# Performance work log

Measured on AMD Instinct MI355X. Metric: run time of the kernel, lower is better.

Reference implementation:

```python
import jax, jax.numpy as jnp
import numpy as np

B, T, DS, N, DR, H, DF, NK, HID = 4, 1024, 1024, 16, 256, 4, 1024, 3, 128
K_VALUES = (1, 2, 4)  # k_values for max_k=4


def _ln(x, scale, bias):
    mu = jnp.mean(x, axis=-1, keepdims=True)
    var = jnp.var(x, axis=-1, keepdims=True)
    return (x - mu) * jax.lax.rsqrt(var + 1e-5) * scale + bias


def setup_inputs() -> dict:
    key = jax.random.key(0)
    ks = jax.random.split(key, 16)
    p = lambda k, shp: 0.02 * jax.random.normal(k, shp, dtype=jnp.float32)
    return {
        "s": jax.random.normal(ks[0], (B, T, DS), dtype=jnp.float32),
        "r": jax.random.normal(ks[1], (B, T, N, DR), dtype=jnp.float32),
        # DifficultyEstimator MLP (d_s -> 128 -> 3 k-logits)
        "Wd1": p(ks[2], (DS, HID)), "bd1": jnp.zeros((HID,), jnp.float32),
        "Wd2": p(ks[3], (HID, NK)), "bd2": jnp.zeros((NK,), jnp.float32),
        # SlotAllocator (r -> hidden -> 1, plus surface projection)
        "Wa1": p(ks[4], (DR, HID)), "ba1": jnp.zeros((HID,), jnp.float32),
        "Wa2": p(ks[5], (HID, 1)), "ba2": jnp.zeros((1,), jnp.float32),
        "Ws": p(ks[6], (DS, 1)),
        # ReasoningStream: masked slot self-attention + FFN
        "ln1_s": jnp.ones((DR,), jnp.float32), "ln1_b": jnp.zeros((DR,), jnp.float32),
        "Wq": p(ks[7], (DR, DR)), "Wk": p(ks[8], (DR, DR)),
        "Wv": p(ks[9], (DR, DR)), "Wo": p(ks[10], (DR, DR)),
        "ln2_s": jnp.ones((DR,), jnp.float32), "ln2_b": jnp.zeros((DR,), jnp.float32),
        "Wf1": p(ks[11], (DR, DF)), "bf1": jnp.zeros((DF,), jnp.float32),
        "Wf2": p(ks[12], (DF, DR)), "bf2": jnp.zeros((DR,), jnp.float32),
    }


def _reasoning_step(r, mask, ln1_s, ln1_b, Wq, Wk, Wv, Wo, ln2_s, ln2_b, Wf1, bf1, Wf2, bf2):
    # one masked update of the per-position slot set: (B,T,N,DR)
    Dh = DR // H
    h = _ln(r, ln1_s, ln1_b)
    q = (h @ Wq).reshape(*h.shape[:-1], H, Dh)
    k = (h @ Wk).reshape(*h.shape[:-1], H, Dh)
    v = (h @ Wv).reshape(*h.shape[:-1], H, Dh)
    scores = jnp.einsum("btnhd,btmhd->bthnm", q, k) / jnp.sqrt(jnp.float32(Dh))
    attn = jax.nn.softmax(scores, axis=-1)
    o = jnp.einsum("bthnm,btmhd->btnhd", attn, v).reshape(r.shape) @ Wo
    r = r + mask * o
    h2 = _ln(r, ln2_s, ln2_b)
    ffn = jax.nn.gelu(h2 @ Wf1 + bf1) @ Wf2 + bf2
    return r + mask * ffn


def reference(s, r, Wd1, bd1, Wd2, bd2, Wa1, ba1, Wa2, ba2, Ws,
              ln1_s, ln1_b, Wq, Wk, Wv, Wo, ln2_s, ln2_b, Wf1, bf1, Wf2, bf2):
    # SlotAllocator: per-position per-slot soft mask (B,T,N,1)
    slot_mask = jax.nn.sigmoid(
        (jax.nn.relu(r @ Wa1 + ba1) @ Wa2 + ba2) + (s @ Ws)[:, :, None, :]
    )
    # DifficultyEstimator: k logits / weights per position (B,T,3)
    k_logits = jax.nn.relu(s @ Wd1 + bd1) @ Wd2 + bd2
    probs = jax.nn.softmax(k_logits, axis=-1)
    k_weights = probs
    # routing balance loss: mse of mean probs vs uniform
    mean_probs = probs.mean(axis=(0, 1))
    routing_loss = jnp.mean((mean_probs - 1.0 / NK) ** 2)
    k_tensor = jnp.asarray(K_VALUES, dtype=s.dtype)
    mean_k = (probs * k_tensor).sum(axis=-1).mean()
    # _combine_adaptive_reasoning (training path): run max_k steps, keep
    # candidates at k in K_VALUES, weighted combine per position.
    step_params = (ln1_s, ln1_b, Wq, Wk, Wv, Wo, ln2_s, ln2_b, Wf1, bf1, Wf2, bf2)
    candidates = []
    r_step = r
    for step in range(1, max(K_VALUES) + 1):
        r_step = _reasoning_step(r_step, slot_mask, *step_params)
        if step in K_VALUES:
            candidates.append(r_step)
    stacked = jnp.stack(candidates, axis=2)  # (B,T,3,N,DR)
    r_out = (k_weights[..., None, None] * stacked).sum(axis=2)
    return r_out, routing_loss, mean_k
```

## Files before the change

kernel.cpp:

```cpp
#include <hip/hip_runtime.h>
#include <hip/hip_bf16.h>
#include <math.h>


#define NPOS 4096
#define R_ELEMS 16777216ull
#define NB 384

typedef __attribute__((ext_vector_type(8))) short short8;
typedef __attribute__((ext_vector_type(4))) float f32x4;

#define MF(a, b, c) __builtin_amdgcn_mfma_f32_16x16x32_bf16(a, b, c, 0, 0, 0)

__device__ __forceinline__ short bf16rne(float f) {
  union { float f; unsigned u; } v; v.f = f;
  unsigned r = v.u + 0x7FFFu + ((v.u >> 16) & 1u);
  return (short)(r >> 16);
}

__device__ __forceinline__ short bf16c(float f) {
  __hip_bfloat16 h = __float2bfloat16(f);
  return *reinterpret_cast<short*>(&h);
}

__device__ __forceinline__ float fast_gelu(float x) {
  float x2 = x * x;
  float z = 0.7978845608028654f * x * (1.f + 0.044715f * x2);
  float e = __expf(2.f * z);
  float t = 1.f - 2.f * __builtin_amdgcn_rcpf(e + 1.f);
  return 0.5f * x * (1.f + t);
}

__global__ void pack_weight(const float* __restrict__ W, short* __restrict__ P,
                            int K, int N) {
  int id = blockIdx.x * 256 + threadIdx.x;
  int KC = K >> 5, T = N >> 4;
  if (id >= T * KC * 64) return;
  int l = id & 63, kc = (id >> 6) % KC, t = id / (64 * KC);
  int g = l >> 4, n = l & 15;
  short8 o;
#pragma unroll
  for (int jj = 0; jj < 8; jj++) {
    int k = 32 * kc + 4 * g + (jj & 3) + 16 * (jj >> 2);
    o[jj] = bf16rne(W[(size_t)k * N + 16 * t + n]);
  }
  *(short8*)(P + (size_t)id * 8) = o;
}

__global__ void pack_stream(const float* __restrict__ Wq, const float* __restrict__ Wk,
                            const float* __restrict__ Wv, const float* __restrict__ Wo,
                            const float* __restrict__ Wf1, const float* __restrict__ Wf2,
                            short* __restrict__ S) {
  int id = blockIdx.x * 256 + threadIdx.x;
  int f = id >> 6, lane = id & 63;
  if (f >= 1536) return;
  const float* W; int ldN, t, kc;
  if (f < 384) {
    int hh = f / 96, rem = f % 96, mat = rem / 32, r2 = rem % 32;
    t = 4 * hh + r2 / 8; kc = r2 % 8; ldN = 256;
    W = (mat == 0) ? Wq : (mat == 1) ? Wk : Wv;
  } else if (f < 512) {
    int gg = f - 384; t = gg / 8; kc = gg % 8; ldN = 256; W = Wo;
  } else {
    int gg = f - 512, hc = gg / 32, r2 = gg % 32;
    if (r2 < 16) { W = Wf1; ldN = 1024; t = 2 * hc + r2 / 8; kc = r2 % 8; }
    else         { W = Wf2; ldN = 256;  t = r2 - 16;         kc = hc;    }
  }
  int g = lane >> 4, n = lane & 15;
  short8 o;
#pragma unroll
  for (int jj = 0; jj < 8; jj++) {
    int k = 32 * kc + 4 * g + (jj & 3) + 16 * (jj >> 2);
    o[jj] = bf16rne(W[(size_t)k * ldN + 16 * t + n]);
  }
  *(short8*)(S + (size_t)f * 512 + lane * 8) = o;
}

__device__ __forceinline__ short8 ldfrag(const short* __restrict__ P, int t, int kc,
                                         int KC, int lane) {
  return *(const short8*)(P + ((size_t)((t * KC + kc) * 64 + lane) << 3));
}

__global__ void init_accum_kernel(float* accum) {
  if (threadIdx.x < 4) accum[threadIdx.x] = 0.f;
}

__global__ void sproj_kernel(const float* __restrict__ s, const float* __restrict__ Ws,
                             float* __restrict__ sproj) {
  int p = blockIdx.x, tid = threadIdx.x;
  const float* row = s + (size_t)p * 1024;
  float sum = 0.f;
#pragma unroll
  for (int k0 = 0; k0 < 1024; k0 += 256) sum += row[k0 + tid] * Ws[k0 + tid];
#pragma unroll
  for (int m = 1; m < 64; m <<= 1) sum += __shfl_xor(sum, m, 64);
  __shared__ float red[4];
  if ((tid & 63) == 0) red[tid >> 6] = sum;
  __syncthreads();
  if (tid == 0) sproj[p] = red[0] + red[1] + red[2] + red[3];
}

__global__ void difficulty_mfma(const float* __restrict__ s, const short* __restrict__ PWd1,
                                const float* __restrict__ bd1, const float* __restrict__ Wd2,
                                const float* __restrict__ bd2, float* __restrict__ probsv,
                                float* __restrict__ accum) {
  int tid = threadIdx.x;
  int wave = tid >> 6, lane = tid & 63, n = lane & 15, g = lane >> 4;
  int p0 = (blockIdx.x * 4 + wave) * 16;
  const float* sg = s + (size_t)(p0 + n) * 1024;
  f32x4 ha[8];
  const f32x4 Z = {0.f, 0.f, 0.f, 0.f};
#pragma unroll
  for (int t = 0; t < 8; t++) ha[t] = Z;
  for (int kc = 0; kc < 32; kc++) {
    f32x4 x0 = *(const f32x4*)(sg + 32 * kc + 4 * g);
    f32x4 x1 = *(const f32x4*)(sg + 32 * kc + 16 + 4 * g);
    short8 sb;
#pragma unroll
    for (int c = 0; c < 4; c++) { sb[c] = bf16c(x0[c]); sb[c + 4] = bf16c(x1[c]); }
#pragma unroll
    for (int t = 0; t < 8; t++) ha[t] = MF(ldfrag(PWd1, t, kc, 32, lane), sb, ha[t]);
  }
  float v0 = 0.f, v1 = 0.f, v2 = 0.f;
#pragma unroll
  for (int t = 0; t < 8; t++)
#pragma unroll
    for (int c = 0; c < 4; c++) {
      int hid = 16 * t + 4 * g + c;
      float u = fmaxf(ha[t][c] + bd1[hid], 0.f);
      v0 += u * Wd2[hid * 3 + 0];
      v1 += u * Wd2[hid * 3 + 1];
      v2 += u * Wd2[hid * 3 + 2];
    }
  v0 += __shfl_xor(v0, 16, 64); v0 += __shfl_xor(v0, 32, 64);
  v1 += __shfl_xor(v1, 16, 64); v1 += __shfl_xor(v1, 32, 64);
  v2 += __shfl_xor(v2, 16, 64); v2 += __shfl_xor(v2, 32, 64);
  if (g == 0) {
    float l0 = v0 + bd2[0], l1 = v1 + bd2[1], l2 = v2 + bd2[2];
    float mx = fmaxf(l0, fmaxf(l1, l2));
    float e0 = __expf(l0 - mx), e1 = __expf(l1 - mx), e2 = __expf(l2 - mx);
    float inv = 1.f / (e0 + e1 + e2);
    float p0v = e0 * inv, p1v = e1 * inv, p2v = e2 * inv;
    int p = p0 + n;
    probsv[p * 3 + 0] = p0v; probsv[p * 3 + 1] = p1v; probsv[p * 3 + 2] = p2v;
    atomicAdd(accum + 0, p0v);
    atomicAdd(accum + 1, p1v);
    atomicAdd(accum + 2, p2v);
    atomicAdd(accum + 3, p0v * 1.f + p1v * 2.f + p2v * 4.f);
  }
}

__global__ void slot_mask_mfma(const float* __restrict__ r, const short* __restrict__ PWa1,
                               const float* __restrict__ ba1, const float* __restrict__ Wa2,
                               const float* __restrict__ ba2, const float* __restrict__ sproj,
                               float* __restrict__ mask) {
  int tid = threadIdx.x;
  int wave = tid >> 6, lane = tid & 63, n = lane & 15, g = lane >> 4;
  int p = blockIdx.x * 4 + wave;
  const float* rsg = r + (size_t)p * 4096 + n * 256;
  short8 rb[8];
#pragma unroll
  for (int kc = 0; kc < 8; kc++) {
    f32x4 x0 = *(const f32x4*)(rsg + 32 * kc + 4 * g);
    f32x4 x1 = *(const f32x4*)(rsg + 32 * kc + 16 + 4 * g);
    short8 o;
#pragma unroll
    for (int c = 0; c < 4; c++) { o[c] = bf16c(x0[c]); o[c + 4] = bf16c(x1[c]); }
    rb[kc] = o;
  }
  f32x4 ha[8];
  const f32x4 Z = {0.f, 0.f, 0.f, 0.f};
#pragma unroll
  for (int t = 0; t < 8; t++) ha[t] = Z;
#pragma unroll
  for (int kc = 0; kc < 8; kc++)
#pragma unroll
    for (int t = 0; t < 8; t++) ha[t] = MF(ldfrag(PWa1, t, kc, 8, lane), rb[kc], ha[t]);
  float v = 0.f;
#pragma unroll
  for (int t = 0; t < 8; t++)
#pragma unroll
    for (int c = 0; c < 4; c++) {
      int hid = 16 * t + 4 * g + c;
      v += fmaxf(ha[t][c] + ba1[hid], 0.f) * Wa2[hid];
    }
  v += __shfl_xor(v, 16, 64);
  v += __shfl_xor(v, 32, 64);
  if (g == 0) mask[p * 16 + n] = 1.f / (1.f + __expf(-(v + ba2[0] + sproj[p])));
}

__global__ __launch_bounds__(256, 2) void reason_all(
    const float* __restrict__ r_src, const float* __restrict__ maskg,
    const float* __restrict__ probsv, float* __restrict__ outp,
    const short* __restrict__ Wstream,
    const float* __restrict__ ln1s, const float* __restrict__ ln1b,
    const float* __restrict__ ln2s, const float* __restrict__ ln2b,
    const float* __restrict__ bf1g, const float* __restrict__ bf2g) {
  __shared__ __align__(16) short Wbuf[4 * 8192];
  __shared__ __align__(16) float P_ln1s[256], P_ln1b[256], P_ln2s[256], P_ln2b[256];
  __shared__ __align__(16) float P_bf1[1024], P_bf2[256];
  const int tid = threadIdx.x;
  P_ln1s[tid] = ln1s[tid]; P_ln1b[tid] = ln1b[tid];
  P_ln2s[tid] = ln2s[tid]; P_ln2b[tid] = ln2b[tid];
  P_bf2[tid] = bf2g[tid];
  for (int i = tid; i < 1024; i += 256) P_bf1[i] = bf1g[i];
  __syncthreads();

  const int wave = tid >> 6, lane = tid & 63;
  const int n = lane & 15, g = lane >> 4;
  const int p = blockIdx.x * 4 + wave;
  const size_t base = (size_t)p * 4096;
  const f32x4 Z = {0.f, 0.f, 0.f, 0.f};

  auto stage_issue = [&](int c) {
    const short* gs = Wstream + (size_t)(c % 96) * 8192 + wave * 2048 + lane * 8;
    short* ld = (short*)Wbuf + (c & 3) * 8192 + wave * 2048;
#pragma unroll
    for (int i = 0; i < 4; ++i)
      __builtin_amdgcn_global_load_lds(
          (const __attribute__((address_space(1))) void*)(gs + i * 512),
          (__attribute__((address_space(3))) void*)(ld + i * 512), 16, 0, 0);
  };
  stage_issue(0); stage_issue(1); stage_issue(2);

  f32x4 r0[8], r1[8];
  {
    const float* rsg = r_src + base + n * 256;
#pragma unroll
    for (int kc = 0; kc < 8; kc++) {
      r0[kc] = *(const f32x4*)(rsg + 32 * kc + 4 * g);
      r1[kc] = *(const f32x4*)(rsg + 32 * kc + 16 + 4 * g);
    }
  }
  const float maskn = maskg[p * 16 + n];
  const float w0 = probsv[p * 3 + 0];
  const float w1 = probsv[p * 3 + 1];
  const float w2 = probsv[p * 3 + 2];

  int cidx = 0;
  auto boundary = [&]() -> const short* {
    int c = cidx++;
    if (c <= NB - 3)
      asm volatile("s_waitcnt vmcnt(8) lgkmcnt(0)\ns_barrier" ::: "memory");
    else if (c == NB - 2)
      asm volatile("s_waitcnt vmcnt(4) lgkmcnt(0)\ns_barrier" ::: "memory");
    else
      asm volatile("s_waitcnt vmcnt(0) lgkmcnt(0)\ns_barrier" ::: "memory");
    __builtin_amdgcn_sched_barrier(0);
    if (c + 3 < NB) stage_issue(c + 3);
    return &Wbuf[(c & 3) * 8192];
  };
#define FRAG(Bp, i) (*(const short8*)((Bp) + (i) * 512 + lane * 8))

  short8 h1[8];
  auto do_ln = [&](const float* sc, const float* bi) {
    float sum = 0.f, sq = 0.f;
#pragma unroll
    for (int kc = 0; kc < 8; kc++)
#pragma unroll
      for (int c = 0; c < 4; c++) {
        sum += r0[kc][c] + r1[kc][c];
        sq += r0[kc][c] * r0[kc][c] + r1[kc][c] * r1[kc][c];
      }
    sum += __shfl_xor(sum, 16, 64); sq += __shfl_xor(sq, 16, 64);
    sum += __shfl_xor(sum, 32, 64); sq += __shfl_xor(sq, 32, 64);
    float mu = sum * (1.f / 256.f);
    float inv = rsqrtf(sq * (1.f / 256.f) - mu * mu + 1e-5f);
#pragma unroll
    for (int kc = 0; kc < 8; kc++) {
      f32x4 s0 = *(const f32x4*)&sc[32 * kc + 4 * g];
      f32x4 b0 = *(const f32x4*)&bi[32 * kc + 4 * g];
      f32x4 s1 = *(const f32x4*)&sc[32 * kc + 16 + 4 * g];
      f32x4 b1 = *(const f32x4*)&bi[32 * kc + 16 + 4 * g];
      short8 hh;
#pragma unroll
      for (int c = 0; c < 4; c++) {
        hh[c]     = bf16c((r0[kc][c] - mu) * inv * s0[c] + b0[c]);
        hh[c + 4] = bf16c((r1[kc][c] - mu) * inv * s1[c] + b1[c]);
      }
      h1[kc] = hh;
    }
  };

  for (int sidx = 0; sidx < 4; ++sidx) {
    do_ln(P_ln1s, P_ln1b);

    short8 ob[8];
#pragma unroll
    for (int hh = 0; hh < 4; hh++) {
      short8 qb[2], kb[2];
      f32x4 va[4];
      {
        f32x4 qa[4];
#pragma unroll
        for (int tp = 0; tp < 2; tp++) {
          const short* B = boundary();
          qa[2 * tp] = Z; qa[2 * tp + 1] = Z;
          __builtin_amdgcn_s_setprio(1);
#pragma unroll
          for (int tt = 0; tt < 2; tt++)
#pragma unroll
            for (int kc = 0; kc < 8; kc++)
              qa[2 * tp + tt] = MF(FRAG(B, tt * 8 + kc), h1[kc], qa[2 * tp + tt]);
          __builtin_amdgcn_s_setprio(0);
        }
#pragma unroll
        for (int c = 0; c < 2; c++) {
          short8 x;
#pragma unroll
          for (int jj = 0; jj < 8; jj++) x[jj] = bf16c(qa[2 * c + (jj >> 2)][jj & 3]);
          qb[c] = x;
        }
      }
      {
        f32x4 ka[4];
#pragma unroll
        for (int tp = 0; tp < 2; tp++) {
          const short* B = boundary();
          ka[2 * tp] = Z; ka[2 * tp + 1] = Z;
          __builtin_amdgcn_s_setprio(1);
#pragma unroll
          for (int tt = 0; tt < 2; tt++)
#pragma unroll
            for (int kc = 0; kc < 8; kc++)
              ka[2 * tp + tt] = MF(FRAG(B, tt * 8 + kc), h1[kc], ka[2 * tp + tt]);
          __builtin_amdgcn_s_setprio(0);
        }
#pragma unroll
        for (int c = 0; c < 2; c++) {
          short8 x;
#pragma unroll
          for (int jj = 0; jj < 8; jj++) x[jj] = bf16c(ka[2 * c + (jj >> 2)][jj & 3]);
          kb[c] = x;
        }
      }
#pragma unroll
      for (int tp = 0; tp < 2; tp++) {
        const short* B = boundary();
        va[2 * tp] = Z; va[2 * tp + 1] = Z;
        __builtin_amdgcn_s_setprio(1);
#pragma unroll
        for (int tt = 0; tt < 2; tt++)
#pragma unroll
          for (int kc = 0; kc < 8; kc++)
            va[2 * tp + tt] = MF(h1[kc], FRAG(B, tt * 8 + kc), va[2 * tp + tt]);
        __builtin_amdgcn_s_setprio(0);
      }
      f32x4 sc = Z;
      sc = MF(kb[0], qb[0], sc);
      sc = MF(kb[1], qb[1], sc);
#pragma unroll
      for (int c = 0; c < 4; c++) sc[c] *= 0.125f;
      float mx = fmaxf(fmaxf(sc[0], sc[1]), fmaxf(sc[2], sc[3]));
      mx = fmaxf(mx, __shfl_xor(mx, 16, 64));
      mx = fmaxf(mx, __shfl_xor(mx, 32, 64));
      float e0 = __expf(sc[0] - mx), e1 = __expf(sc[1] - mx);
      float e2 = __expf(sc[2] - mx), e3 = __expf(sc[3] - mx);
      float sm = e0 + e1 + e2 + e3;
      sm += __shfl_xor(sm, 16, 64);
      sm += __shfl_xor(sm, 32, 64);
      float isv = __builtin_amdgcn_rcpf(sm);
      short8 pb;
      pb[0] = bf16c(e0 * isv); pb[1] = bf16c(e1 * isv);
      pb[2] = bf16c(e2 * isv); pb[3] = bf16c(e3 * isv);
      pb[4] = 0; pb[5] = 0; pb[6] = 0; pb[7] = 0;
      short8 vb[4];
#pragma unroll
      for (int t = 0; t < 4; t++) {
        short8 x;
        x[0] = bf16c(va[t][0]); x[1] = bf16c(va[t][1]);
        x[2] = bf16c(va[t][2]); x[3] = bf16c(va[t][3]);
        x[4] = 0; x[5] = 0; x[6] = 0; x[7] = 0;
        vb[t] = x;
      }
      f32x4 oh[4];
#pragma unroll
      for (int t = 0; t < 4; t++) { oh[t] = Z; oh[t] = MF(vb[t], pb, oh[t]); }
#pragma unroll
      for (int c = 0; c < 2; c++) {
        short8 x;
#pragma unroll
        for (int jj = 0; jj < 8; jj++)
          x[jj] = bf16c(maskn * oh[2 * c + (jj >> 2)][jj & 3]);
        ob[2 * hh + c] = x;
      }
    }

#pragma unroll
    for (int kk = 0; kk < 8; kk++) {
      const short* B = boundary();
      __builtin_amdgcn_s_setprio(1);
#pragma unroll
      for (int kc = 0; kc < 8; kc++) r0[kk] = MF(FRAG(B, kc), ob[kc], r0[kk]);
#pragma unroll
      for (int kc = 0; kc < 8; kc++) r1[kk] = MF(FRAG(B, 8 + kc), ob[kc], r1[kk]);
      __builtin_amdgcn_s_setprio(0);
    }

    do_ln(P_ln2s, P_ln2b);
#pragma unroll 1
    for (int hc = 0; hc < 32; hc++) {
      f32x4 ht0 = Z, ht1 = Z;
      {
        const short* B = boundary();
        __builtin_amdgcn_s_setprio(1);
#pragma unroll
        for (int kc = 0; kc < 8; kc++) ht0 = MF(FRAG(B, kc), h1[kc], ht0);
#pragma unroll
        for (int kc = 0; kc < 8; kc++) ht1 = MF(FRAG(B, 8 + kc), h1[kc], ht1);
        __builtin_amdgcn_s_setprio(0);
      }
      f32x4 u0 = *(const f32x4*)&P_bf1[32 * hc + 4 * g];
      f32x4 u1 = *(const f32x4*)&P_bf1[32 * hc + 16 + 4 * g];
      short8 hbb;
#pragma unroll
      for (int c = 0; c < 4; c++) {
        hbb[c]     = bf16c(maskn * fast_gelu(ht0[c] + u0[c]));
        hbb[c + 4] = bf16c(maskn * fast_gelu(ht1[c] + u1[c]));
      }
      {
        const short* B = boundary();
        __builtin_amdgcn_s_setprio(1);
#pragma unroll
        for (int tt = 0; tt < 8; tt++) {
          r0[tt] = MF(FRAG(B, 2 * tt), hbb, r0[tt]);
          r1[tt] = MF(FRAG(B, 2 * tt + 1), hbb, r1[tt]);
        }
        __builtin_amdgcn_s_setprio(0);
      }
    }
#pragma unroll
    for (int kc = 0; kc < 8; kc++) {
      f32x4 b0 = *(const f32x4*)&P_bf2[32 * kc + 4 * g];
      f32x4 b1 = *(const f32x4*)&P_bf2[32 * kc + 16 + 4 * g];
#pragma unroll
      for (int c = 0; c < 4; c++) {
        r0[kc][c] += maskn * b0[c];
        r1[kc][c] += maskn * b1[c];
      }
    }

    if (sidx == 0) {
      float* op = outp + base + n * 256;
#pragma unroll
      for (int kc = 0; kc < 8; kc++) {
        f32x4 o0, o1;
#pragma unroll
        for (int c = 0; c < 4; c++) { o0[c] = w0 * r0[kc][c]; o1[c] = w0 * r1[kc][c]; }
        *(f32x4*)(op + 32 * kc + 4 * g) = o0;
        *(f32x4*)(op + 32 * kc + 16 + 4 * g) = o1;
      }
    } else if (sidx == 1 || sidx == 3) {
      float wc = (sidx == 1) ? w1 : w2;
      float* op = outp + base + n * 256;
#pragma unroll
      for (int kc = 0; kc < 8; kc++) {
        f32x4 o0 = *(f32x4*)(op + 32 * kc + 4 * g);
        f32x4 o1 = *(f32x4*)(op + 32 * kc + 16 + 4 * g);
#pragma unroll
        for (int c = 0; c < 4; c++) { o0[c] += wc * r0[kc][c]; o1[c] += wc * r1[kc][c]; }
        *(f32x4*)(op + 32 * kc + 4 * g) = o0;
        *(f32x4*)(op + 32 * kc + 16 + 4 * g) = o1;
      }
    }
  }
}

__global__ void finalize_kernel(const float* __restrict__ accum, float* __restrict__ dst) {
  const float inv = 1.f / 4096.f;
  float m0 = accum[0] * inv, m1 = accum[1] * inv, m2 = accum[2] * inv;
  const float u = 1.f / 3.f;
  float d0 = m0 - u, d1 = m1 - u, d2 = m2 - u;
  dst[0] = (d0 * d0 + d1 * d1 + d2 * d2) * (1.f / 3.f);
  dst[1] = accum[3] * inv;
}

extern "C" void kernel_launch(void* const* d_in, const int* in_sizes, int n_in,
                              void* d_out, int out_size, void* d_ws, size_t ws_size,
                              hipStream_t stream) {
  const float* s    = (const float*)d_in[0];
  const float* r    = (const float*)d_in[1];
  const float* Wd1  = (const float*)d_in[2];
  const float* bd1  = (const float*)d_in[3];
  const float* Wd2  = (const float*)d_in[4];
  const float* bd2  = (const float*)d_in[5];
  const float* Wa1  = (const float*)d_in[6];
  const float* ba1  = (const float*)d_in[7];
  const float* Wa2  = (const float*)d_in[8];
  const float* ba2  = (const float*)d_in[9];
  const float* Wsp  = (const float*)d_in[10];
  const float* ln1s = (const float*)d_in[11];
  const float* ln1b = (const float*)d_in[12];
  const float* Wq   = (const float*)d_in[13];
  const float* Wk   = (const float*)d_in[14];
  const float* Wv   = (const float*)d_in[15];
  const float* Wo   = (const float*)d_in[16];
  const float* ln2s = (const float*)d_in[17];
  const float* ln2b = (const float*)d_in[18];
  const float* Wf1  = (const float*)d_in[19];
  const float* bf1  = (const float*)d_in[20];
  const float* Wf2  = (const float*)d_in[21];
  const float* bf2  = (const float*)d_in[22];

  float* out = (float*)d_out;
  float* wsf = (float*)d_ws;
  float* mask   = wsf;
  float* sproj  = wsf + 65536;
  float* probsv = wsf + 65536 + 4096;
  float* accum  = wsf + 65536 + 4096 + 12288;
  short* pk     = (short*)(wsf + 131072);
  short* Wstream = pk;
  short* PWa1    = pk + 786432;
  short* PWd1    = pk + 819200;

  pack_stream<<<384, 256, 0, stream>>>(Wq, Wk, Wv, Wo, Wf1, Wf2, Wstream);
  pack_weight<<<16, 256, 0, stream>>>(Wa1, PWa1, 256, 128);
  pack_weight<<<64, 256, 0, stream>>>(Wd1, PWd1, 1024, 128);

  init_accum_kernel<<<1, 64, 0, stream>>>(accum);
  sproj_kernel<<<NPOS, 256, 0, stream>>>(s, Wsp, sproj);
  difficulty_mfma<<<64, 256, 0, stream>>>(s, PWd1, bd1, Wd2, bd2, probsv, accum);
  slot_mask_mfma<<<NPOS / 4, 256, 0, stream>>>(r, PWa1, ba1, Wa2, ba2, sproj, mask);

  reason_all<<<NPOS / 4, 256, 0, stream>>>(r, mask, probsv, out, Wstream,
                                           ln1s, ln1b, ln2s, ln2b, bf1, bf2);

  finalize_kernel<<<1, 1, 0, stream>>>(accum, out + R_ELEMS);
}
```

Baseline: 705.4 us.

## Process two positions per wave to reuse each staged weight fragment twice

Each wave now handles two positions (A and B) and applies every LDS weight fragment to both, which halves the grid and the total weight streaming through LDS per position. The Wo projection is interleaved per head, with the weight stream reordered to match, so the attention output can be consumed right after each head instead of buffering all heads. This doubles the accumulator register footprint (four r arrays), which can cut occupancy or cause spills, and the loops are left at unroll 1.

```diff
diff --git a/kernel.cpp b/kernel.cpp
--- a/kernel.cpp
+++ b/kernel.cpp
@@ -55,16 +55,24 @@
   int f = id >> 6, lane = id & 63;
   if (f >= 1536) return;
   const float* W; int ldN, t, kc;
-  if (f < 384) {
-    int hh = f / 96, rem = f % 96, mat = rem / 32, r2 = rem % 32;
-    t = 4 * hh + r2 / 8; kc = r2 % 8; ldN = 256;
-    W = (mat == 0) ? Wq : (mat == 1) ? Wk : Wv;
-  } else if (f < 512) {
-    int gg = f - 384; t = gg / 8; kc = gg % 8; ldN = 256; W = Wo;
+  if (f < 512) {
+    int head = f >> 7, rem = f & 127;
+    if (rem < 96) {
+      int mat = rem / 32, r2 = rem % 32;
+      t = 4 * head + (r2 >> 3);
+      kc = r2 & 7; ldN = 256;
+      W = (mat == 0) ? Wq : (mat == 1) ? Wk : Wv;
+    } else {
+      int r2 = rem - 96;
+      int ch = r2 >> 4, floc = r2 & 15;
+      t = ch * 8 + (floc >> 1);
+      kc = 2 * head + (floc & 1);
+      ldN = 256; W = Wo;
+    }
   } else {
     int gg = f - 512, hc = gg / 32, r2 = gg % 32;
-    if (r2 < 16) { W = Wf1; ldN = 1024; t = 2 * hc + r2 / 8; kc = r2 % 8; }
-    else         { W = Wf2; ldN = 256;  t = r2 - 16;         kc = hc;    }
+    if (r2 < 16) { W = Wf1; ldN = 1024; t = 2 * hc + (r2 >> 3); kc = r2 & 7; }
+    else         { W = Wf2; ldN = 256;  t = r2 - 16;            kc = hc;    }
   }
   int g = lane >> 4, n = lane & 15;
   short8 o;
@@ -208,8 +216,8 @@
 
   const int wave = tid >> 6, lane = tid & 63;
   const int n = lane & 15, g = lane >> 4;
-  const int p = blockIdx.x * 4 + wave;
-  const size_t base = (size_t)p * 4096;
+  const int pA = blockIdx.x * 8 + wave * 2, pB = pA + 1;
+  const size_t baseA = (size_t)pA * 4096, baseB = (size_t)pB * 4096;
   const f32x4 Z = {0.f, 0.f, 0.f, 0.f};
 
   auto stage_issue = [&](int c) {
@@ -223,19 +231,20 @@
   };
   stage_issue(0); stage_issue(1); stage_issue(2);
 
-  f32x4 r0[8], r1[8];
+  f32x4 rA0[8], rA1[8], rB0[8], rB1[8];
   {
-    const float* rsg = r_src + base + n * 256;
+    const float* ra = r_src + baseA + n * 256;
+    const float* rb = r_src + baseB + n * 256;
 #pragma unroll
     for (int kc = 0; kc < 8; kc++) {
-      r0[kc] = *(const f32x4*)(rsg + 32 * kc + 4 * g);
-      r1[kc] = *(const f32x4*)(rsg + 32 * kc + 16 + 4 * g);
-    }
-  }
-  const float maskn = maskg[p * 16 + n];
-  const float w0 = probsv[p * 3 + 0];
-  const float w1 = probsv[p * 3 + 1];
-  const float w2 = probsv[p * 3 + 2];
+      rA0[kc] = *(const f32x4*)(ra + 32 * kc + 4 * g);
+      rA1[kc] = *(const f32x4*)(ra + 32 * kc + 16 + 4 * g);
+      rB0[kc] = *(const f32x4*)(rb + 32 * kc + 4 * g);
+      rB1[kc] = *(const f32x4*)(rb + 32 * kc + 16 + 4 * g);
+    }
+  }
+  const float maskA = maskg[pA * 16 + n];
+  const float maskB = maskg[pB * 16 + n];
 
   int cidx = 0;
   auto boundary = [&]() -> const short* {
@@ -252,8 +261,9 @@
   };
 #define FRAG(Bp, i) (*(const short8*)((Bp) + (i) * 512 + lane * 8))
 
-  short8 h1[8];
-  auto do_ln = [&](const float* sc, const float* bi) {
+  short8 hA[8], hB[8];
+  auto do_ln = [&](const f32x4* r0, const f32x4* r1, const float* sc,
+                   const float* bi, short8* h) {
     float sum = 0.f, sq = 0.f;
 #pragma unroll
     for (int kc = 0; kc < 8; kc++)
@@ -278,153 +288,197 @@
         hh[c]     = bf16c((r0[kc][c] - mu) * inv * s0[c] + b0[c]);
         hh[c + 4] = bf16c((r1[kc][c] - mu) * inv * s1[c] + b1[c]);
       }
-      h1[kc] = hh;
+      h[kc] = hh;
     }
   };
 
+#pragma unroll 1
   for (int sidx = 0; sidx < 4; ++sidx) {
-    do_ln(P_ln1s, P_ln1b);
-
-    short8 ob[8];
-#pragma unroll
-    for (int hh = 0; hh < 4; hh++) {
-      short8 qb[2], kb[2];
-      f32x4 va[4];
+    do_ln(rA0, rA1, P_ln1s, P_ln1b, hA);
+    do_ln(rB0, rB1, P_ln1s, P_ln1b, hB);
+
+#pragma unroll 1
+    for (int hh = 0; hh < 4; ++hh) {
+      short8 qbA[2], qbB[2], kbA[2], kbB[2];
+#pragma unroll
+      for (int tp = 0; tp < 2; ++tp) {
+        const short* Bp = boundary();
+        f32x4 a0A = Z, a1A = Z, a0B = Z, a1B = Z;
+        __builtin_amdgcn_s_setprio(1);
+#pragma unroll
+        for (int kc = 0; kc < 8; kc++) {
+          short8 fr = FRAG(Bp, kc);
+          a0A = MF(fr, hA[kc], a0A); a0B = MF(fr, hB[kc], a0B);
+        }
+#pragma unroll
+        for (int kc = 0; kc < 8; kc++) {
+          short8 fr = FRAG(Bp, 8 + kc);
+          a1A = MF(fr, hA[kc], a1A); a1B = MF(fr, hB[kc], a1B);
+        }
+        __builtin_amdgcn_s_setprio(0);
+        short8 xA, xB;
+#pragma unroll
+        for (int jj = 0; jj < 8; jj++) {
+          xA[jj] = bf16c(jj < 4 ? a0A[jj & 3] : a1A[jj & 3]);
+          xB[jj] = bf16c(jj < 4 ? a0B[jj & 3] : a1B[jj & 3]);
+        }
+        qbA[tp] = xA; qbB[tp] = xB;
+      }
+#pragma unroll
+      for (int tp = 0; tp < 2; ++tp) {
+        const short* Bp = boundary();
+        f32x4 a0A = Z, a1A = Z, a0B = Z, a1B = Z;
+        __builtin_amdgcn_s_setprio(1);
+#pragma unroll
+        for (int kc = 0; kc < 8; kc++) {
+          short8 fr = FRAG(Bp, kc);
+          a0A = MF(fr, hA[kc], a0A); a0B = MF(fr, hB[kc], a0B);
+        }
+#pragma unroll
+        for (int kc = 0; kc < 8; kc++) {
+          short8 fr = FRAG(Bp, 8 + kc);
+          a1A = MF(fr, hA[kc], a1A); a1B = MF(fr, hB[kc], a1B);
+        }
+        __builtin_amdgcn_s_setprio(0);
+        short8 xA, xB;
+#pragma unroll
+        for (int jj = 0; jj < 8; jj++) {
+          xA[jj] = bf16c(jj < 4 ? a0A[jj & 3] : a1A[jj & 3]);
+          xB[jj] = bf16c(jj < 4 ? a0B[jj & 3] : a1B[jj & 3]);
+        }
+        kbA[tp] = xA; kbB[tp] = xB;
+      }
+      short8 pbA, pbB;
       {
-        f32x4 qa[4];
-#pragma unroll
-        for (int tp = 0; tp < 2; tp++) {
-          const short* B = boundary();
-          qa[2 * tp] = Z; qa[2 * tp + 1] = Z;
-          __builtin_amdgcn_s_setprio(1);
-#pragma unroll
-          for (int tt = 0; tt < 2; tt++)
-#pragma unroll
-            for (int kc = 0; kc < 8; kc++)
-              qa[2 * tp + tt] = MF(FRAG(B, tt * 8 + kc), h1[kc], qa[2 * tp + tt]);
-          __builtin_amdgcn_s_setprio(0);
-        }
-#pragma unroll
-        for (int c = 0; c < 2; c++) {
-          short8 x;
-#pragma unroll
-          for (int jj = 0; jj < 8; jj++) x[jj] = bf16c(qa[2 * c + (jj >> 2)][jj & 3]);
-          qb[c] = x;
-        }
+        f32x4 sc1 = Z;
+        sc1 = MF(kbA[0], qbA[0], sc1);
+        sc1 = MF(kbA[1], qbA[1], sc1);
+#pragma unroll
+        for (int c = 0; c < 4; c++) sc1[c] *= 0.125f;
+        float mx = fmaxf(fmaxf(sc1[0], sc1[1]), fmaxf(sc1[2], sc1[3]));
+        mx = fmaxf(mx, __shfl_xor(mx, 16, 64));
+        mx = fmaxf(mx, __shfl_xor(mx, 32, 64));
+        float e0 = __expf(sc1[0] - mx), e1 = __expf(sc1[1] - mx);
+        float e2 = __expf(sc1[2] - mx), e3 = __expf(sc1[3] - mx);
+        float sm = e0 + e1 + e2 + e3;
+        sm += __shfl_xor(sm, 16, 64);
+        sm += __shfl_xor(sm, 32, 64);
+        float isv = __builtin_amdgcn_rcpf(sm);
+        pbA[0] = bf16c(e0 * isv); pbA[1] = bf16c(e1 * isv);
+        pbA[2] = bf16c(e2 * isv); pbA[3] = bf16c(e3 * isv);
+        pbA[4] = 0; pbA[5] = 0; pbA[6] = 0; pbA[7] = 0;
       }
       {
-        f32x4 ka[4];
-#pragma unroll
-        for (int tp = 0; tp < 2; tp++) {
-          const short* B = boundary();
-          ka[2 * tp] = Z; ka[2 * tp + 1] = Z;
-          __builtin_amdgcn_s_setprio(1);
-#pragma unroll
-          for (int tt = 0; tt < 2; tt++)
-#pragma unroll
-            for (int kc = 0; kc < 8; kc++)
-              ka[2 * tp + tt] = MF(FRAG(B, tt * 8 + kc), h1[kc], ka[2 * tp + tt]);
-          __builtin_amdgcn_s_setprio(0);
-        }
-#pragma unroll
-        for (int c = 0; c < 2; c++) {
-          short8 x;
-#pragma unroll
-          for (int jj = 0; jj < 8; jj++) x[jj] = bf16c(ka[2 * c + (jj >> 2)][jj & 3]);
-          kb[c] = x;
-        }
-      }
-#pragma unroll
-      for (int tp = 0; tp < 2; tp++) {
-        const short* B = boundary();
-        va[2 * tp] = Z; va[2 * tp + 1] = Z;
+        f32x4 sc1 = Z;
+        sc1 = MF(kbB[0], qbB[0], sc1);
+        sc1 = MF(kbB[1], qbB[1], sc1);
+#pragma unroll
+        for (int c = 0; c < 4; c++) sc1[c] *= 0.125f;
+        float mx = fmaxf(fmaxf(sc1[0], sc1[1]), fmaxf(sc1[2], sc1[3]));
+        mx = fmaxf(mx, __shfl_xor(mx, 16, 64));
+        mx = fmaxf(mx, __shfl_xor(mx, 32, 64));
+        float e0 = __expf(sc1[0] - mx), e1 = __expf(sc1[1] - mx);
+        float e2 = __expf(sc1[2] - mx), e3 = __expf(sc1[3] - mx);
+        float sm = e0 + e1 + e2 + e3;
+        sm += __shfl_xor(sm, 16, 64);
+        sm += __shfl_xor(sm, 32, 64);
+        float isv = __builtin_amdgcn_rcpf(sm);
+        pbB[0] = bf16c(e0 * isv); pbB[1] = bf16c(e1 * isv);
+        pbB[2] = bf16c(e2 * isv); pbB[3] = bf16c(e3 * isv);
+        pbB[4] = 0; pbB[5] = 0; pbB[6] = 0; pbB[7] = 0;
+      }
+      short8 osA[2], osB[2];
+#pragma unroll
+      for (int tp = 0; tp < 2; ++tp) {
+        const short* Bp = boundary();
+        f32x4 v0A = Z, v1A = Z, v0B = Z, v1B = Z;
         __builtin_amdgcn_s_setprio(1);
 #pragma unroll
-        for (int tt = 0; tt < 2; tt++)
-#pragma unroll
-          for (int kc = 0; kc < 8; kc++)
-            va[2 * tp + tt] = MF(h1[kc], FRAG(B, tt * 8 + kc), va[2 * tp + tt]);
+        for (int kc = 0; kc < 8; kc++) {
+          short8 fr = FRAG(Bp, kc);
+          v0A = MF(hA[kc], fr, v0A); v0B = MF(hB[kc], fr, v0B);
+        }
+#pragma unroll
+        for (int kc = 0; kc < 8; kc++) {
+          short8 fr = FRAG(Bp, 8 + kc);
+          v1A = MF(hA[kc], fr, v1A); v1B = MF(hB[kc], fr, v1B);
+        }
         __builtin_amdgcn_s_setprio(0);
-      }
-      f32x4 sc = Z;
-      sc = MF(kb[0], qb[0], sc);
-      sc = MF(kb[1], qb[1], sc);
-#pragma unroll
-      for (int c = 0; c < 4; c++) sc[c] *= 0.125f;
-      float mx = fmaxf(fmaxf(sc[0], sc[1]), fmaxf(sc[2], sc[3]));
-      mx = fmaxf(mx, __shfl_xor(mx, 16, 64));
-      mx = fmaxf(mx, __shfl_xor(mx, 32, 64));
-      float e0 = __expf(sc[0] - mx), e1 = __expf(sc[1] - mx);
-      float e2 = __expf(sc[2] - mx), e3 = __expf(sc[3] - mx);
-      float sm = e0 + e1 + e2 + e3;
-      sm += __shfl_xor(sm, 16, 64);
-      sm += __shfl_xor(sm, 32, 64);
-      float isv = __builtin_amdgcn_rcpf(sm);
-      short8 pb;
-      pb[0] = bf16c(e0 * isv); pb[1] = bf16c(e1 * isv);
-      pb[2] = bf16c(e2 * isv); pb[3] = bf16c(e3 * isv);
-      pb[4] = 0; pb[5] = 0; pb[6] = 0; pb[7] = 0;
-      short8 vb[4];
-#pragma unroll
-      for (int t = 0; t < 4; t++) {
-        short8 x;
-        x[0] = bf16c(va[t][0]); x[1] = bf16c(va[t][1]);
-        x[2] = bf16c(va[t][2]); x[3] = bf16c(va[t][3]);
-        x[4] = 0; x[5] = 0; x[6] = 0; x[7] = 0;
-        vb[t] = x;
-      }
-      f32x4 oh[4];
-#pragma unroll
-      for (int t = 0; t < 4; t++) { oh[t] = Z; oh[t] = MF(vb[t], pb, oh[t]); }
-#pragma unroll
-      for (int c = 0; c < 2; c++) {
-        short8 x;
-#pragma unroll
-        for (int jj = 0; jj < 8; jj++)
-          x[jj] = bf16c(maskn * oh[2 * c + (jj >> 2)][jj & 3]);
-        ob[2 * hh + c] = x;
-      }
-    }
-
-#pragma unroll
-    for (int kk = 0; kk < 8; kk++) {
-      const short* B = boundary();
-      __builtin_amdgcn_s_setprio(1);
-#pragma unroll
-      for (int kc = 0; kc < 8; kc++) r0[kk] = MF(FRAG(B, kc), ob[kc], r0[kk]);
-#pragma unroll
-      for (int kc = 0; kc < 8; kc++) r1[kk] = MF(FRAG(B, 8 + kc), ob[kc], r1[kk]);
-      __builtin_amdgcn_s_setprio(0);
-    }
-
-    do_ln(P_ln2s, P_ln2b);
+        short8 vb0A, vb1A, vb0B, vb1B;
+#pragma unroll
+        for (int c = 0; c < 4; c++) {
+          vb0A[c] = bf16c(v0A[c]); vb1A[c] = bf16c(v1A[c]);
+          vb0B[c] = bf16c(v0B[c]); vb1B[c] = bf16c(v1B[c]);
+          vb0A[c + 4] = 0; vb1A[c + 4] = 0; vb0B[c + 4] = 0; vb1B[c + 4] = 0;
+        }
+        f32x4 oh0A = MF(vb0A, pbA, Z), oh1A = MF(vb1A, pbA, Z);
+        f32x4 oh0B = MF(vb0B, pbB, Z), oh1B = MF(vb1B, pbB, Z);
+        short8 yA, yB;
+#pragma unroll
+        for (int jj = 0; jj < 8; jj++) {
+          yA[jj] = bf16c(maskA * (jj < 4 ? oh0A[jj & 3] : oh1A[jj & 3]));
+          yB[jj] = bf16c(maskB * (jj < 4 ? oh0B[jj & 3] : oh1B[jj & 3]));
+        }
+        osA[tp] = yA; osB[tp] = yB;
+      }
+#pragma unroll
+      for (int ch = 0; ch < 2; ++ch) {
+        const short* Bp = boundary();
+        __builtin_amdgcn_s_setprio(1);
+#pragma unroll
+        for (int tloc = 0; tloc < 8; ++tloc) {
+          short8 f0 = FRAG(Bp, 2 * tloc), f1 = FRAG(Bp, 2 * tloc + 1);
+          int kk = ch * 4 + (tloc >> 1);
+          if ((tloc & 1) == 0) {
+            rA0[kk] = MF(f0, osA[0], rA0[kk]); rA0[kk] = MF(f1, osA[1], rA0[kk]);
+            rB0[kk] = MF(f0, osB[0], rB0[kk]); rB0[kk] = MF(f1, osB[1], rB0[kk]);
+          } else {
+            rA1[kk] = MF(f0, osA[0], rA1[kk]); rA1[kk] = MF(f1, osA[1], rA1[kk]);
+            rB1[kk] = MF(f0, osB[0], rB1[kk]); rB1[kk] = MF(f1, osB[1], rB1[kk]);
+          }
+        }
+        __builtin_amdgcn_s_setprio(0);
+      }
+    }
+
+    do_ln(rA0, rA1, P_ln2s, P_ln2b, hA);
+    do_ln(rB0, rB1, P_ln2s, P_ln2b, hB);
 #pragma unroll 1
     for (int hc = 0; hc < 32; hc++) {
-      f32x4 ht0 = Z, ht1 = Z;
+      f32x4 t0A = Z, t1A = Z, t0B = Z, t1B = Z;
       {
-        const short* B = boundary();
+        const short* Bp = boundary();
         __builtin_amdgcn_s_setprio(1);
 #pragma unroll
-        for (int kc = 0; kc < 8; kc++) ht0 = MF(FRAG(B, kc), h1[kc], ht0);
-#pragma unroll
-        for (int kc = 0; kc < 8; kc++) ht1 = MF(FRAG(B, 8 + kc), h1[kc], ht1);
+        for (int kc = 0; kc < 8; kc++) {
+          short8 fr = FRAG(Bp, kc);
+          t0A = MF(fr, hA[kc], t0A); t0B = MF(fr, hB[kc], t0B);
+        }
+#pragma unroll
+        for (int kc = 0; kc < 8; kc++) {
+          short8 fr = FRAG(Bp, 8 + kc);
+          t1A = MF(fr, hA[kc], t1A); t1B = MF(fr, hB[kc], t1B);
+        }
         __builtin_amdgcn_s_setprio(0);
       }
       f32x4 u0 = *(const f32x4*)&P_bf1[32 * hc + 4 * g];
       f32x4 u1 = *(const f32x4*)&P_bf1[32 * hc + 16 + 4 * g];
-      short8 hbb;
+      short8 hbbA, hbbB;
 #pragma unroll
       for (int c = 0; c < 4; c++) {
-        hbb[c]     = bf16c(maskn * fast_gelu(ht0[c] + u0[c]));
-        hbb[c + 4] = bf16c(maskn * fast_gelu(ht1[c] + u1[c]));
+        hbbA[c]     = bf16c(maskA * fast_gelu(t0A[c] + u0[c]));
+        hbbA[c + 4] = bf16c(maskA * fast_gelu(t1A[c] + u1[c]));
+        hbbB[c]     = bf16c(maskB * fast_gelu(t0B[c] + u0[c]));
+        hbbB[c + 4] = bf16c(maskB * fast_gelu(t1B[c] + u1[c]));
       }
       {
-        const short* B = boundary();
+        const short* Bp = boundary();
         __builtin_amdgcn_s_setprio(1);
 #pragma unroll
         for (int tt = 0; tt < 8; tt++) {
-          r0[tt] = MF(FRAG(B, 2 * tt), hbb, r0[tt]);
-          r1[tt] = MF(FRAG(B, 2 * tt + 1), hbb, r1[tt]);
+          short8 f0 = FRAG(Bp, 2 * tt), f1 = FRAG(Bp, 2 * tt + 1);
+          rA0[tt] = MF(f0, hbbA, rA0[tt]); rB0[tt] = MF(f0, hbbB, rB0[tt]);
+          rA1[tt] = MF(f1, hbbA, rA1[tt]); rB1[tt] = MF(f1, hbbB, rB1[tt]);
         }
         __builtin_amdgcn_s_setprio(0);
       }
@@ -435,32 +489,48 @@
       f32x4 b1 = *(const f32x4*)&P_bf2[32 * kc + 16 + 4 * g];
 #pragma unroll
       for (int c = 0; c < 4; c++) {
-        r0[kc][c] += maskn * b0[c];
-        r1[kc][c] += maskn * b1[c];
+        rA0[kc][c] += maskA * b0[c]; rA1[kc][c] += maskA * b1[c];
+        rB0[kc][c] += maskB * b0[c]; rB1[kc][c] += maskB * b1[c];
       }
     }
 
     if (sidx == 0) {
-      float* op = outp + base + n * 256;
+      float wa = probsv[pA * 3 + 0], wb = probsv[pB * 3 + 0];
+      float* oa = outp + baseA + n * 256;
+      float* ob2 = outp + baseB + n * 256;
 #pragma unroll
       for (int kc = 0; kc < 8; kc++) {
-        f32x4 o0, o1;
-#pragma unroll
-        for (int c = 0; c < 4; c++) { o0[c] = w0 * r0[kc][c]; o1[c] = w0 * r1[kc][c]; }
-        *(f32x4*)(op + 32 * kc + 4 * g) = o0;
-        *(f32x4*)(op + 32 * kc + 16 + 4 * g) = o1;
+        f32x4 xa0, xa1, xb0, xb1;
+#pragma unroll
+        for (int c = 0; c < 4; c++) {
+          xa0[c] = wa * rA0[kc][c]; xa1[c] = wa * rA1[kc][c];
+          xb0[c] = wb * rB0[kc][c]; xb1[c] = wb * rB1[kc][c];
+        }
+        *(f32x4*)(oa + 32 * kc + 4 * g) = xa0;
+        *(f32x4*)(oa + 32 * kc + 16 + 4 * g) = xa1;
+        *(f32x4*)(ob2 + 32 * kc + 4 * g) = xb0;
+        *(f32x4*)(ob2 + 32 * kc + 16 + 4 * g) = xb1;
       }
     } else if (sidx == 1 || sidx == 3) {
-      float wc = (sidx == 1) ? w1 : w2;
-      float* op = outp + base + n * 256;
+      int ci = (sidx == 1) ? 1 : 2;
+      float wa = probsv[pA * 3 + ci], wb = probsv[pB * 3 + ci];
+      float* oa = outp + baseA + n * 256;
+      float* ob2 = outp + baseB + n * 256;
 #pragma unroll
       for (int kc = 0; kc < 8; kc++) {
-        f32x4 o0 = *(f32x4*)(op + 32 * kc + 4 * g);
-        f32x4 o1 = *(f32x4*)(op + 32 * kc + 16 + 4 * g);
-#pragma unroll
-        for (int c = 0; c < 4; c++) { o0[c] += wc * r0[kc][c]; o1[c] += wc * r1[kc][c]; }
-        *(f32x4*)(op + 32 * kc + 4 * g) = o0;
-        *(f32x4*)(op + 32 * kc + 16 + 4 * g) = o1;
+        f32x4 xa0 = *(f32x4*)(oa + 32 * kc + 4 * g);
+        f32x4 xa1 = *(f32x4*)(oa + 32 * kc + 16 + 4 * g);
+        f32x4 xb0 = *(f32x4*)(ob2 + 32 * kc + 4 * g);
+        f32x4 xb1 = *(f32x4*)(ob2 + 32 * kc + 16 + 4 * g);
+#pragma unroll
+        for (int c = 0; c < 4; c++) {
+          xa0[c] += wa * rA0[kc][c]; xa1[c] += wa * rA1[kc][c];
+          xb0[c] += wb * rB0[kc][c]; xb1[c] += wb * rB1[kc][c];
+        }
+        *(f32x4*)(oa + 32 * kc + 4 * g) = xa0;
+        *(f32x4*)(oa + 32 * kc + 16 + 4 * g) = xa1;
+        *(f32x4*)(ob2 + 32 * kc + 4 * g) = xb0;
+        *(f32x4*)(ob2 + 32 * kc + 16 + 4 * g) = xb1;
       }
     }
   }
@@ -522,7 +592,7 @@
   difficulty_mfma<<<64, 256, 0, stream>>>(s, PWd1, bd1, Wd2, bd2, probsv, accum);
   slot_mask_mfma<<<NPOS / 4, 256, 0, stream>>>(r, PWa1, ba1, Wa2, ba2, sproj, mask);
 
-  reason_all<<<NPOS / 4, 256, 0, stream>>>(r, mask, probsv, out, Wstream,
+  reason_all<<<NPOS / 8, 256, 0, stream>>>(r, mask, probsv, out, Wstream,
                                            ln1s, ln1b, ln2s, ln2b, bf1, bf2);
 
   finalize_kernel<<<1, 1, 0, stream>>>(accum, out + R_ELEMS);
```

After: 604.2 us. -14.4%, faster.
